# Kernel tuning notes

Measured on AMD Instinct MI355X. Metric: run time of the kernel, lower is better.

Reference implementation:

```python
import jax, jax.numpy as jnp
import numpy as np

NUM_CLASSES = 1000  # label vocabulary size (matches fill_max for label)
B = 16384
D_IN = 1024   # image_embedding
D_OUT = 256   # projection_dim


def setup_inputs() -> dict:
    key = jax.random.key(0)
    k = jax.random.split(key, 6)
    x = jax.random.normal(k[0], (B, D_IN), dtype=jnp.float32)
    label = jax.random.randint(k[1], (B,), 0, NUM_CLASSES, dtype=jnp.int64)
    scale = 1.0 / np.sqrt(D_IN)
    W1_w = jax.random.normal(k[2], (D_OUT, D_IN), dtype=jnp.float32) * scale
    W1_b = jax.random.normal(k[3], (D_OUT,), dtype=jnp.float32) * scale
    W2_w = jax.random.normal(k[4], (D_OUT, D_IN), dtype=jnp.float32) * scale
    W2_b = jax.random.normal(k[5], (D_OUT,), dtype=jnp.float32) * scale
    return {"x": x, "label": label, "W1_w": W1_w, "W1_b": W1_b,
            "W2_w": W2_w, "W2_b": W2_b}


def reference(x, label, W1_w, W1_b, W2_w, W2_b):
    # Leave-one-group-out mean, vectorized via segment sums.
    # Original: for each i, mean of x[label != label_i] (detached); zeros if none.
    b = x.shape[0]
    xd = jax.lax.stop_gradient(x)  # .detach() in the torch code
    label_sum = jax.ops.segment_sum(xd, label, num_segments=NUM_CLASSES)          # [C, D_IN]
    label_cnt = jax.ops.segment_sum(jnp.ones((b,), dtype=x.dtype), label,
                                    num_segments=NUM_CLASSES)                     # [C]
    total_sum = xd.sum(axis=0)                                                    # [D_IN]
    other_sum = total_sum[None, :] - label_sum[label]                             # [B, D_IN]
    other_cnt = jnp.asarray(b, x.dtype) - label_cnt[label]                        # [B]
    calculate_mean = jnp.where(other_cnt[:, None] > 0,
                               other_sum / jnp.maximum(other_cnt, 1)[:, None],
                               jnp.zeros((), x.dtype))                            # [B, D_IN]
    # W1(x) + W2(calculate_mean)  (torch Linear: y = x @ W.T + b)
    return x @ W1_w.T + W1_b + calculate_mean @ W2_w.T + W2_b
```

## Files before the change

### kernel.cpp

```cpp
#include <hip/hip_runtime.h>

constexpr int B      = 16384;
constexpr int D_IN   = 1024;
constexpr int D_OUT  = 256;
constexpr int NCLS   = 1000;

constexpr size_t OFF_WB  = 0;
constexpr size_t OFF_XB  = OFF_WB + (size_t)512 * D_IN * 2;
constexpr size_t OFF_V   = OFF_XB + (size_t)B * D_IN * 2;
constexpr size_t OFF_U   = OFF_V  + (size_t)1024 * D_OUT * 4;
constexpr size_t OFF_CNT = OFF_U  + 4096;
constexpr size_t OFF_B12 = OFF_CNT + 4096;

typedef short bf16x8 __attribute__((ext_vector_type(8)));
typedef float f32x4  __attribute__((ext_vector_type(4)));

__device__ __forceinline__ unsigned short f2bf(float f) {
    unsigned int u = __float_as_uint(f);
    return (unsigned short)((u + 0x7FFFu + ((u >> 16) & 1u)) >> 16);
}

__device__ __forceinline__ void cvt8(const float4& a, const float4& b, unsigned short* dst) {
    union { unsigned short u[8]; bf16x8 v; } r;
    r.u[0] = f2bf(a.x); r.u[1] = f2bf(a.y); r.u[2] = f2bf(a.z); r.u[3] = f2bf(a.w);
    r.u[4] = f2bf(b.x); r.u[5] = f2bf(b.y); r.u[6] = f2bf(b.z); r.u[7] = f2bf(b.w);
    *(bf16x8*)dst = r.v;
}

__device__ __forceinline__ unsigned int cvtpk(float lo, float hi) {
    unsigned int r;
    asm volatile("v_cvt_pk_bf16_f32 %0, %1, %2" : "=v"(r) : "v"(lo), "v"(hi));
    return r;
}

__device__ __forceinline__ void async16(const unsigned short* g, unsigned short* l) {
    __builtin_amdgcn_global_load_lds(
        (const __attribute__((address_space(1))) void*)g,
        (__attribute__((address_space(3))) void*)l,
        16, 0, 0);
}

__global__ __launch_bounds__(256)
void prep_kernel(const float* __restrict__ W1, const float* __restrict__ W2,
                 const float* __restrict__ b1, const float* __restrict__ b2,
                 const int* __restrict__ label,
                 unsigned short* __restrict__ Wb,
                 float* __restrict__ V, float* __restrict__ U,
                 int* __restrict__ cnt, float* __restrict__ b12) {
    const int blk = blockIdx.x, tid = threadIdx.x;
    if (blk == 0) {
        __shared__ int h[1024];
#pragma unroll
        for (int q = 0; q < 4; ++q) h[q * 256 + tid] = 0;
        __syncthreads();
        for (int base = 0; base < 64; base += 16) {
            int lv[16];
#pragma unroll
            for (int u = 0; u < 16; ++u) lv[u] = label[(base + u) * 256 + tid];
#pragma unroll
            for (int u = 0; u < 16; ++u) atomicAdd(&h[lv[u]], 1);
        }
        __syncthreads();
#pragma unroll
        for (int q = 0; q < 4; ++q) cnt[q * 256 + tid] = h[q * 256 + tid];
        b12[tid] = b1[tid] + b2[tid];
    } else if (blk <= 128) {
        int lin = (blk - 1) * 256 + tid;
        int i = lin * 16;
        const float* src = (i < D_OUT * D_IN) ? (W1 + i) : (W2 + (i - D_OUT * D_IN));
        float4 a0 = *(const float4*)(src);
        float4 a1 = *(const float4*)(src + 4);
        float4 a2 = *(const float4*)(src + 8);
        float4 a3 = *(const float4*)(src + 12);
        cvt8(a0, a1, Wb + i);
        cvt8(a2, a3, Wb + i + 8);
    } else {
        int lb = blk - 129;
        int base = (lb * 256 + tid) * 16;
#pragma unroll
        for (int q = 0; q < 4; ++q)
            *(float4*)(V + base + q * 4) = float4{0.f, 0.f, 0.f, 0.f};
        if (lb == 0 && tid < 64)
            *(float4*)(U + tid * 4) = float4{0.f, 0.f, 0.f, 0.f};
    }
}

__global__ __launch_bounds__(256, 2)
void gemm2_kernel(const float* __restrict__ x,
                  const unsigned short* __restrict__ Wb,
                  const int* __restrict__ label,
                  unsigned short* __restrict__ xb,
                  float* __restrict__ V, float* __restrict__ U) {
    __shared__ unsigned short As[2][128][64];
    __shared__ unsigned short Bs[2][64][64];

    const int tid  = threadIdx.x;
    const int bid  = blockIdx.x;
    const int xcd   = bid & 7;
    const int local = bid >> 3;
    const int bx = xcd * 16 + (local & 15);
    const int by = local >> 4;
    const int bm = bx * 128;
    const int bn = by * 64;

    const int wave = tid >> 6, lane = tid & 63;
    const int quad = lane >> 4, l16 = lane & 15;
    const int wm = (wave >> 1) * 64;
    const int wn = (wave & 1) * 32;
    const int sx = l16 & 7;

    const float* xps[4];
    unsigned short* xbp[4];
    int adst[4];
#pragma unroll
    for (int rr = 0; rr < 4; ++rr) {
        int dd = rr * 256 + tid;
        int r = dd >> 3, sl = dd & 7;
        int sc = sl ^ (r & 7);
        xps[rr] = x  + (size_t)(bm + r) * D_IN + sc * 8;
        xbp[rr] = xb + (size_t)(bm + r) * D_IN + sc * 8;
        adst[rr] = dd * 8;
    }
    const unsigned short* bps[2];
#pragma unroll
    for (int rr = 0; rr < 2; ++rr) {
        int dd = rr * 256 + tid;
        int r = dd >> 3, sl = dd & 7;
        int sc = sl ^ (r & 7);
        bps[rr] = Wb + (size_t)(256 + bn + r) * D_IN + sc * 8;
    }
    const bool emit = (by == 0);

    f32x4 acc[4][2] = {};
    float4 a0[4], a1[4];

#pragma unroll
    for (int rr = 0; rr < 4; ++rr) {
        a0[rr] = *(const float4*)(xps[rr]);
        a1[rr] = *(const float4*)(xps[rr] + 4);
    }
#pragma unroll
    for (int rr = 0; rr < 2; ++rr)
        async16(bps[rr], &Bs[0][0][0] + rr * 2048 + wave * 512);
#pragma unroll
    for (int rr = 0; rr < 4; ++rr) {
        union { unsigned int w[4]; bf16x8 v; } p;
        p.w[0] = cvtpk(a0[rr].x, a0[rr].y);
        p.w[1] = cvtpk(a0[rr].z, a0[rr].w);
        p.w[2] = cvtpk(a1[rr].x, a1[rr].y);
        p.w[3] = cvtpk(a1[rr].z, a1[rr].w);
        *(bf16x8*)(&As[0][0][0] + adst[rr]) = p.v;
        if (emit) *(bf16x8*)(xbp[rr]) = p.v;
    }

    for (int t = 0; t < 16; ++t) {
        const int cur = t & 1;
        const int k1 = (t + 1) * 64;
        if (t < 15) {
#pragma unroll
            for (int rr = 0; rr < 4; ++rr) {
                a0[rr] = *(const float4*)(xps[rr] + k1);
                a1[rr] = *(const float4*)(xps[rr] + k1 + 4);
            }
            asm volatile("s_waitcnt vmcnt(8)" ::: "memory");
        } else {
            asm volatile("s_waitcnt vmcnt(0)" ::: "memory");
        }
        asm volatile("s_waitcnt lgkmcnt(0)" ::: "memory");
        __builtin_amdgcn_s_barrier();
        __builtin_amdgcn_sched_barrier(0);
        if (t < 15) {
#pragma unroll
            for (int rr = 0; rr < 2; ++rr)
                async16(bps[rr] + k1, &Bs[cur ^ 1][0][0] + rr * 2048 + wave * 512);
        }

#pragma unroll
        for (int ks = 0; ks < 2; ++ks) {
            const int s = ks * 4 + quad;
            bf16x8 af[4], bfr[2];
#pragma unroll
            for (int i = 0; i < 4; ++i)
                af[i] = *(const bf16x8*)&As[cur][wm + i * 16 + l16][((s ^ sx) * 8)];
#pragma unroll
            for (int j = 0; j < 2; ++j)
                bfr[j] = *(const bf16x8*)&Bs[cur][wn + j * 16 + l16][((s ^ sx) * 8)];
#pragma unroll
            for (int i = 0; i < 4; ++i)
#pragma unroll
                for (int j = 0; j < 2; ++j)
                    acc[i][j] = __builtin_amdgcn_mfma_f32_16x16x32_bf16(af[i], bfr[j], acc[i][j], 0, 0, 0);
        }

        if (t < 15) {
#pragma unroll
            for (int rr = 0; rr < 4; ++rr) {
                union { unsigned int w[4]; bf16x8 v; } p;
                p.w[0] = cvtpk(a0[rr].x, a0[rr].y);
                p.w[1] = cvtpk(a0[rr].z, a0[rr].w);
                p.w[2] = cvtpk(a1[rr].x, a1[rr].y);
                p.w[3] = cvtpk(a1[rr].z, a1[rr].w);
                *(bf16x8*)(&As[cur ^ 1][0][0] + adst[rr]) = p.v;
                if (emit) *(bf16x8*)(xbp[rr] + k1) = p.v;
            }
        }
    }

    int lab[4][4];
#pragma unroll
    for (int i = 0; i < 4; ++i)
#pragma unroll
        for (int r = 0; r < 4; ++r)
            lab[i][r] = label[bm + wm + i * 16 + quad * 4 + r] * D_OUT;

#pragma unroll
    for (int j = 0; j < 2; ++j) {
        const int n = bn + wn + j * 16 + l16;
        float cs = 0.f;
#pragma unroll
        for (int i = 0; i < 4; ++i)
#pragma unroll
            for (int r = 0; r < 4; ++r) {
                float v = acc[i][j][r];
                cs += v;
                atomicAdd(&V[lab[i][r] + n], v);
            }
        cs += __shfl_xor(cs, 16);
        cs += __shfl_xor(cs, 32);
        if (quad == 0) atomicAdd(&U[n], cs);
    }
}

__global__ __launch_bounds__(256)
void gemm1_kernel(const unsigned short* __restrict__ xb,
                  const unsigned short* __restrict__ Wb,
                  const int* __restrict__ label,
                  const float* __restrict__ V, const float* __restrict__ U,
                  const int* __restrict__ cnt, const float* __restrict__ b12,
                  float* __restrict__ out) {
    __shared__ unsigned short As[128][64];
    __shared__ unsigned short Bs[64][64];

    const int tid  = threadIdx.x;
    const int bid  = blockIdx.x;
    const int xcd   = bid & 7;
    const int local = bid >> 3;
    const int bx = xcd * 16 + (local & 15);
    const int by = local >> 4;
    const int bm = bx * 128;
    const int bn = by * 64;

    const int wave = tid >> 6, lane = tid & 63;
    const int quad = lane >> 4, l16 = lane & 15;
    const int wm = (wave >> 1) * 64;
    const int wn = (wave & 1) * 32;
    const int sx = l16 & 7;

    const unsigned short* aps[4];
#pragma unroll
    for (int rr = 0; rr < 4; ++rr) {
        int dd = rr * 256 + tid;
        int r = dd >> 3, sl = dd & 7;
        int sc = sl ^ (r & 7);
        aps[rr] = xb + (size_t)(bm + r) * D_IN + sc * 8;
    }
    const unsigned short* bps[2];
#pragma unroll
    for (int rr = 0; rr < 2; ++rr) {
        int dd = rr * 256 + tid;
        int r = dd >> 3, sl = dd & 7;
        int sc = sl ^ (r & 7);
        bps[rr] = Wb + (size_t)(bn + r) * D_IN + sc * 8;
    }

    f32x4 acc[4][2] = {};

    for (int k0 = 0; k0 < D_IN; k0 += 64) {
        __syncthreads();
#pragma unroll
        for (int rr = 0; rr < 4; ++rr)
            async16(aps[rr] + k0, &As[0][0] + rr * 2048 + wave * 512);
#pragma unroll
        for (int rr = 0; rr < 2; ++rr)
            async16(bps[rr] + k0, &Bs[0][0] + rr * 2048 + wave * 512);
        __syncthreads();

#pragma unroll
        for (int ks = 0; ks < 2; ++ks) {
            const int s = ks * 4 + quad;
            bf16x8 af[4], bfr[2];
#pragma unroll
            for (int i = 0; i < 4; ++i)
                af[i] = *(const bf16x8*)&As[wm + i * 16 + l16][((s ^ sx) * 8)];
#pragma unroll
            for (int j = 0; j < 2; ++j)
                bfr[j] = *(const bf16x8*)&Bs[wn + j * 16 + l16][((s ^ sx) * 8)];
#pragma unroll
            for (int i = 0; i < 4; ++i)
#pragma unroll
                for (int j = 0; j < 2; ++j)
                    acc[i][j] = __builtin_amdgcn_mfma_f32_16x16x32_bf16(af[i], bfr[j], acc[i][j], 0, 0, 0);
        }
    }

    int lab[4][4];
    float inv[4][4];
#pragma unroll
    for (int i = 0; i < 4; ++i)
#pragma unroll
        for (int r = 0; r < 4; ++r) {
            const int m = bm + wm + i * 16 + quad * 4 + r;
            const int L = label[m];
            lab[i][r] = L * D_OUT;
            inv[i][r] = 1.0f / (float)(B - cnt[L]);
        }

#pragma unroll
    for (int j = 0; j < 2; ++j) {
        const int n = bn + wn + j * 16 + l16;
        const float un = U[n];
        const float bb = b12[n];
#pragma unroll
        for (int i = 0; i < 4; ++i)
#pragma unroll
            for (int r = 0; r < 4; ++r) {
                const int m = bm + wm + i * 16 + quad * 4 + r;
                out[(size_t)m * D_OUT + n] =
                    acc[i][j][r] + bb + (un - V[lab[i][r] + n]) * inv[i][r];
            }
    }
}

extern "C" void kernel_launch(void* const* d_in, const int* in_sizes, int n_in,
                              void* d_out, int out_size, void* d_ws, size_t ws_size,
                              hipStream_t stream) {
    const float* x    = (const float*)d_in[0];
    const int*   lab  = (const int*)d_in[1];
    const float* W1_w = (const float*)d_in[2];
    const float* W1_b = (const float*)d_in[3];
    const float* W2_w = (const float*)d_in[4];
    const float* W2_b = (const float*)d_in[5];
    float* out = (float*)d_out;

    char* ws = (char*)d_ws;
    unsigned short* Wb = (unsigned short*)(ws + OFF_WB);
    unsigned short* xb = (unsigned short*)(ws + OFF_XB);
    float* V   = (float*)(ws + OFF_V);
    float* U   = (float*)(ws + OFF_U);
    int*   cnt = (int*)(ws + OFF_CNT);
    float* b12 = (float*)(ws + OFF_B12);

    prep_kernel<<<193, 256, 0, stream>>>(W1_w, W2_w, W1_b, W2_b, lab, Wb, V, U, cnt, b12);
    gemm2_kernel<<<512, 256, 0, stream>>>(x, Wb, lab, xb, V, U);
    gemm1_kernel<<<512, 256, 0, stream>>>(xb, Wb, lab, V, U, cnt, b12, out);
}
```

Before: 155.5 us.

## Load fp32 x directly into LDS in both GEMMs, drop bf16 x staging buffer

Both GEMM kernels now stream fp32 x straight into LDS through async global-to-LDS loads and convert to bf16 while reading MFMA fragments. This removes the intermediate bf16 copy of x that gemm2 used to write and gemm1 read back. gemm2 also drops its register-prefetch double buffering for a simpler single-buffered loop with two barriers per step. The cost is twice the fp32 traffic for x (read by both kernels), larger LDS tiles, and conversion work repeated in every wave that touches a tile.

```diff
diff --git a/kernel.cpp b/kernel.cpp
--- a/kernel.cpp
+++ b/kernel.cpp
@@ -6,8 +6,7 @@
 constexpr int NCLS   = 1000;
 
 constexpr size_t OFF_WB  = 0;
-constexpr size_t OFF_XB  = OFF_WB + (size_t)512 * D_IN * 2;
-constexpr size_t OFF_V   = OFF_XB + (size_t)B * D_IN * 2;
+constexpr size_t OFF_V   = OFF_WB + (size_t)512 * D_IN * 2;
 constexpr size_t OFF_U   = OFF_V  + (size_t)1024 * D_OUT * 4;
 constexpr size_t OFF_CNT = OFF_U  + 4096;
 constexpr size_t OFF_B12 = OFF_CNT + 4096;
@@ -33,11 +32,20 @@
     return r;
 }
 
-__device__ __forceinline__ void async16(const unsigned short* g, unsigned short* l) {
+__device__ __forceinline__ void async16(const void* g, void* l) {
     __builtin_amdgcn_global_load_lds(
         (const __attribute__((address_space(1))) void*)g,
         (__attribute__((address_space(3))) void*)l,
         16, 0, 0);
+}
+
+__device__ __forceinline__ bf16x8 packfrag(const float4& f0, const float4& f1) {
+    union { unsigned int w[4]; bf16x8 v; } p;
+    p.w[0] = cvtpk(f0.x, f0.y);
+    p.w[1] = cvtpk(f0.z, f0.w);
+    p.w[2] = cvtpk(f1.x, f1.y);
+    p.w[3] = cvtpk(f1.z, f1.w);
+    return p.v;
 }
 
 __global__ __launch_bounds__(256)
@@ -85,14 +93,14 @@
     }
 }
 
-__global__ __launch_bounds__(256, 2)
+
+__global__ __launch_bounds__(256)
 void gemm2_kernel(const float* __restrict__ x,
                   const unsigned short* __restrict__ Wb,
                   const int* __restrict__ label,
-                  unsigned short* __restrict__ xb,
                   float* __restrict__ V, float* __restrict__ U) {
-    __shared__ unsigned short As[2][128][64];
-    __shared__ unsigned short Bs[2][64][64];
+    __shared__ float Asf[128][64];
+    __shared__ unsigned short Bs[64][64];
 
     const int tid  = threadIdx.x;
     const int bid  = blockIdx.x;
@@ -109,17 +117,13 @@
     const int wn = (wave & 1) * 32;
     const int sx = l16 & 7;
 
-    const float* xps[4];
-    unsigned short* xbp[4];
-    int adst[4];
-#pragma unroll
-    for (int rr = 0; rr < 4; ++rr) {
+    const float* aps[8];
+#pragma unroll
+    for (int rr = 0; rr < 8; ++rr) {
         int dd = rr * 256 + tid;
-        int r = dd >> 3, sl = dd & 7;
-        int sc = sl ^ (r & 7);
-        xps[rr] = x  + (size_t)(bm + r) * D_IN + sc * 8;
-        xbp[rr] = xb + (size_t)(bm + r) * D_IN + sc * 8;
-        adst[rr] = dd * 8;
+        int r = dd >> 4, sl = dd & 15;
+        int sc = sl ^ (r & 15);
+        aps[rr] = x + (size_t)(bm + r) * D_IN + sc * 4;
     }
     const unsigned short* bps[2];
 #pragma unroll
@@ -129,80 +133,38 @@
         int sc = sl ^ (r & 7);
         bps[rr] = Wb + (size_t)(256 + bn + r) * D_IN + sc * 8;
     }
-    const bool emit = (by == 0);
 
     f32x4 acc[4][2] = {};
-    float4 a0[4], a1[4];
-
-#pragma unroll
-    for (int rr = 0; rr < 4; ++rr) {
-        a0[rr] = *(const float4*)(xps[rr]);
-        a1[rr] = *(const float4*)(xps[rr] + 4);
-    }
-#pragma unroll
-    for (int rr = 0; rr < 2; ++rr)
-        async16(bps[rr], &Bs[0][0][0] + rr * 2048 + wave * 512);
-#pragma unroll
-    for (int rr = 0; rr < 4; ++rr) {
-        union { unsigned int w[4]; bf16x8 v; } p;
-        p.w[0] = cvtpk(a0[rr].x, a0[rr].y);
-        p.w[1] = cvtpk(a0[rr].z, a0[rr].w);
-        p.w[2] = cvtpk(a1[rr].x, a1[rr].y);
-        p.w[3] = cvtpk(a1[rr].z, a1[rr].w);
-        *(bf16x8*)(&As[0][0][0] + adst[rr]) = p.v;
-        if (emit) *(bf16x8*)(xbp[rr]) = p.v;
-    }
-
-    for (int t = 0; t < 16; ++t) {
-        const int cur = t & 1;
-        const int k1 = (t + 1) * 64;
-        if (t < 15) {
-#pragma unroll
-            for (int rr = 0; rr < 4; ++rr) {
-                a0[rr] = *(const float4*)(xps[rr] + k1);
-                a1[rr] = *(const float4*)(xps[rr] + k1 + 4);
-            }
-            asm volatile("s_waitcnt vmcnt(8)" ::: "memory");
-        } else {
-            asm volatile("s_waitcnt vmcnt(0)" ::: "memory");
-        }
-        asm volatile("s_waitcnt lgkmcnt(0)" ::: "memory");
-        __builtin_amdgcn_s_barrier();
-        __builtin_amdgcn_sched_barrier(0);
-        if (t < 15) {
-#pragma unroll
-            for (int rr = 0; rr < 2; ++rr)
-                async16(bps[rr] + k1, &Bs[cur ^ 1][0][0] + rr * 2048 + wave * 512);
-        }
+
+    for (int k0 = 0; k0 < D_IN; k0 += 64) {
+        __syncthreads();
+#pragma unroll
+        for (int rr = 0; rr < 8; ++rr)
+            async16(aps[rr] + k0, (char*)&Asf[0][0] + rr * 4096 + wave * 1024);
+#pragma unroll
+        for (int rr = 0; rr < 2; ++rr)
+            async16(bps[rr] + k0, (char*)&Bs[0][0] + rr * 4096 + wave * 1024);
+        __syncthreads();
 
 #pragma unroll
         for (int ks = 0; ks < 2; ++ks) {
             const int s = ks * 4 + quad;
             bf16x8 af[4], bfr[2];
 #pragma unroll
-            for (int i = 0; i < 4; ++i)
-                af[i] = *(const bf16x8*)&As[cur][wm + i * 16 + l16][((s ^ sx) * 8)];
+            for (int i = 0; i < 4; ++i) {
+                const int row = wm + i * 16 + l16;
+                float4 f0 = *(const float4*)&Asf[row][((2 * s) ^ l16) * 4];
+                float4 f1 = *(const float4*)&Asf[row][((2 * s + 1) ^ l16) * 4];
+                af[i] = packfrag(f0, f1);
+            }
 #pragma unroll
             for (int j = 0; j < 2; ++j)
-                bfr[j] = *(const bf16x8*)&Bs[cur][wn + j * 16 + l16][((s ^ sx) * 8)];
+                bfr[j] = *(const bf16x8*)&Bs[wn + j * 16 + l16][((s ^ sx) * 8)];
 #pragma unroll
             for (int i = 0; i < 4; ++i)
 #pragma unroll
                 for (int j = 0; j < 2; ++j)
                     acc[i][j] = __builtin_amdgcn_mfma_f32_16x16x32_bf16(af[i], bfr[j], acc[i][j], 0, 0, 0);
-        }
-
-        if (t < 15) {
-#pragma unroll
-            for (int rr = 0; rr < 4; ++rr) {
-                union { unsigned int w[4]; bf16x8 v; } p;
-                p.w[0] = cvtpk(a0[rr].x, a0[rr].y);
-                p.w[1] = cvtpk(a0[rr].z, a0[rr].w);
-                p.w[2] = cvtpk(a1[rr].x, a1[rr].y);
-                p.w[3] = cvtpk(a1[rr].z, a1[rr].w);
-                *(bf16x8*)(&As[cur ^ 1][0][0] + adst[rr]) = p.v;
-                if (emit) *(bf16x8*)(xbp[rr] + k1) = p.v;
-            }
         }
     }
 
@@ -232,13 +194,13 @@
 }
 
 __global__ __launch_bounds__(256)
-void gemm1_kernel(const unsigned short* __restrict__ xb,
+void gemm1_kernel(const float* __restrict__ x,
                   const unsigned short* __restrict__ Wb,
                   const int* __restrict__ label,
                   const float* __restrict__ V, const float* __restrict__ U,
                   const int* __restrict__ cnt, const float* __restrict__ b12,
                   float* __restrict__ out) {
-    __shared__ unsigned short As[128][64];
+    __shared__ float Asf[128][64];
     __shared__ unsigned short Bs[64][64];
 
     const int tid  = threadIdx.x;
@@ -256,13 +218,13 @@
     const int wn = (wave & 1) * 32;
     const int sx = l16 & 7;
 
-    const unsigned short* aps[4];
-#pragma unroll
-    for (int rr = 0; rr < 4; ++rr) {
+    const float* aps[8];
+#pragma unroll
+    for (int rr = 0; rr < 8; ++rr) {
         int dd = rr * 256 + tid;
-        int r = dd >> 3, sl = dd & 7;
-        int sc = sl ^ (r & 7);
-        aps[rr] = xb + (size_t)(bm + r) * D_IN + sc * 8;
+        int r = dd >> 4, sl = dd & 15;
+        int sc = sl ^ (r & 15);
+        aps[rr] = x + (size_t)(bm + r) * D_IN + sc * 4;
     }
     const unsigned short* bps[2];
 #pragma unroll
@@ -278,11 +240,11 @@
     for (int k0 = 0; k0 < D_IN; k0 += 64) {
         __syncthreads();
 #pragma unroll
-        for (int rr = 0; rr < 4; ++rr)
-            async16(aps[rr] + k0, &As[0][0] + rr * 2048 + wave * 512);
+        for (int rr = 0; rr < 8; ++rr)
+            async16(aps[rr] + k0, (char*)&Asf[0][0] + rr * 4096 + wave * 1024);
 #pragma unroll
         for (int rr = 0; rr < 2; ++rr)
-            async16(bps[rr] + k0, &Bs[0][0] + rr * 2048 + wave * 512);
+            async16(bps[rr] + k0, (char*)&Bs[0][0] + rr * 4096 + wave * 1024);
         __syncthreads();
 
 #pragma unroll
@@ -290,8 +252,12 @@
             const int s = ks * 4 + quad;
             bf16x8 af[4], bfr[2];
 #pragma unroll
-            for (int i = 0; i < 4; ++i)
-                af[i] = *(const bf16x8*)&As[wm + i * 16 + l16][((s ^ sx) * 8)];
+            for (int i = 0; i < 4; ++i) {
+                const int row = wm + i * 16 + l16;
+                float4 f0 = *(const float4*)&Asf[row][((2 * s) ^ l16) * 4];
+                float4 f1 = *(const float4*)&Asf[row][((2 * s + 1) ^ l16) * 4];
+                af[i] = packfrag(f0, f1);
+            }
 #pragma unroll
             for (int j = 0; j < 2; ++j)
                 bfr[j] = *(const bf16x8*)&Bs[wn + j * 16 + l16][((s ^ sx) * 8)];
@@ -344,13 +310,12 @@
 
     char* ws = (char*)d_ws;
     unsigned short* Wb = (unsigned short*)(ws + OFF_WB);
-    unsigned short* xb = (unsigned short*)(ws + OFF_XB);
     float* V   = (float*)(ws + OFF_V);
     float* U   = (float*)(ws + OFF_U);
     int*   cnt = (int*)(ws + OFF_CNT);
     float* b12 = (float*)(ws + OFF_B12);
 
     prep_kernel<<<193, 256, 0, stream>>>(W1_w, W2_w, W1_b, W2_b, lab, Wb, V, U, cnt, b12);
-    gemm2_kernel<<<512, 256, 0, stream>>>(x, Wb, lab, xb, V, U);
-    gemm1_kernel<<<512, 256, 0, stream>>>(xb, Wb, lab, V, U, cnt, b12, out);
-}
+    gemm2_kernel<<<512, 256, 0, stream>>>(x, Wb, lab, V, U);
+    gemm1_kernel<<<512, 256, 0, stream>>>(x, Wb, lab, V, U, cnt, b12, out);
+}
```

Measured after the change: 162.4 us. 4.4% more time.
